# Optimization experiments

Measured on AMD Instinct MI355X. Metric: run time of the kernel, lower is better.

The kernel has to match this reference:

```python
import jax, jax.numpy as jnp
import numpy as np

N = 50000      # nodes
E = 800000     # edges (before self-loops)
IN = 128       # in_channels
HID = 32       # hidden_channels per head
H = 4          # in_head
OUT = 40       # out_channels
OH = 1         # out_head
NEG = 0.2      # GATConv default negative_slope
EPS = 1e-5     # BatchNorm eps
SKIP = 0.5     # skip_coefficient


def setup_inputs() -> dict:
    key = jax.random.key(0)
    ks = jax.random.split(key, 24)
    s = 0.1
    f32 = jnp.float32
    return dict(
        x=jax.random.normal(ks[0], (N, IN), dtype=f32),
        W0=jax.random.normal(ks[1], (H * HID, IN), dtype=f32) * s,
        as0=jax.random.normal(ks[2], (H, HID), dtype=f32) * s,
        ad0=jax.random.normal(ks[3], (H, HID), dtype=f32) * s,
        b0=jnp.zeros((H * HID,), f32),
        g0=jnp.ones((H * HID,), f32),
        be0=jnp.zeros((H * HID,), f32),
        W1=jax.random.normal(ks[4], (H * HID, H * HID), dtype=f32) * s,
        as1=jax.random.normal(ks[5], (H, HID), dtype=f32) * s,
        ad1=jax.random.normal(ks[6], (H, HID), dtype=f32) * s,
        b1=jnp.zeros((H * HID,), f32),
        g1=jnp.ones((H * HID,), f32),
        be1=jnp.zeros((H * HID,), f32),
        W2=jax.random.normal(ks[7], (OH * OUT, H * HID), dtype=f32) * s,
        as2=jax.random.normal(ks[8], (OH, OUT), dtype=f32) * s,
        ad2=jax.random.normal(ks[9], (OH, OUT), dtype=f32) * s,
        b2=jnp.zeros((OH * OUT,), f32),
        edge_index=jax.random.randint(ks[10], (2, E), 0, N, dtype=jnp.int64),
    )


def gat_layer(x, src, dst, W, a_s, a_d, b, heads, ch):
    # PyG GATConv (concat=True): per-head linear, edge LeakyReLU attention,
    # softmax over incoming edges per destination node, scatter-add aggregate.
    n = x.shape[0]
    h = (x @ W.T).reshape(n, heads, ch)            # [N,H,C]
    al_s = jnp.einsum('nhc,hc->nh', h, a_s)        # [N,H]
    al_d = jnp.einsum('nhc,hc->nh', h, a_d)
    e = jax.nn.leaky_relu(al_s[src] + al_d[dst], NEG)   # [Etot,H]
    m = jax.ops.segment_max(e, dst, num_segments=n)     # per-dst max (stable softmax)
    ex = jnp.exp(e - m[dst])
    denom = jax.ops.segment_sum(ex, dst, num_segments=n)
    alpha = ex / denom[dst]                              # [Etot,H]
    out = jax.ops.segment_sum(alpha[:, :, None] * h[src], dst, num_segments=n)
    return out.reshape(n, heads * ch) + b


def batchnorm(x, g, b):
    # BatchNorm1d, batch-statistics form
    mu = x.mean(0)
    var = x.var(0)
    return (x - mu) * jax.lax.rsqrt(var + EPS) * g + b


def reference(x, W0, as0, ad0, b0, g0, be0, W1, as1, ad1, b1, g1, be1,
              W2, as2, ad2, b2, edge_index):
    loops = jnp.arange(N, dtype=edge_index.dtype)   # GATConv add_self_loops=True
    src = jnp.concatenate([edge_index[0], loops])
    dst = jnp.concatenate([edge_index[1], loops])
    h = jax.nn.relu(batchnorm(gat_layer(x, src, dst, W0, as0, ad0, b0, H, HID), g0, be0))
    skip = h
    h = gat_layer(h, src, dst, W1, as1, ad1, b1, H, HID)
    h = jax.nn.relu(batchnorm(h, g1, be1) + SKIP * skip)
    return gat_layer(h, src, dst, W2, as2, ad2, b2, OH, OUT)
```

## Files before the change

### kernel.cpp

```cpp
#include <hip/hip_runtime.h>
#include <hip/hip_bf16.h>
#include <stdint.h>

#define N_NODES 50000
#define N_EDGES 800000
#define TOT_EDGES (N_EDGES + N_NODES)
#define DIM 128
#define NEG 0.2f
#define BN_EPS 1e-5f
#define SKIPC 0.5f
#define NB 196
#define BCAP 6144
#define EPB 2048
#define BINA_BLKS ((N_EDGES + EPB - 1) / EPB)

typedef __attribute__((ext_vector_type(8))) short short8;
typedef __attribute__((ext_vector_type(4))) float f32x4;

__device__ inline float bf2f(__hip_bfloat16 v) { return __bfloat162float(v); }
__device__ inline float u16f(unsigned short u) { return __uint_as_float(((unsigned int)u) << 16); }
__device__ inline unsigned short f2bu(float f) {
    __hip_bfloat16 b = __float2bfloat16(f);
    return *(unsigned short*)&b;
}
__device__ inline void fma8(float* acc, float ex, uint4 u) {
    acc[0] += ex * u16f((unsigned short)(u.x & 0xFFFFu));
    acc[1] += ex * u16f((unsigned short)(u.x >> 16));
    acc[2] += ex * u16f((unsigned short)(u.y & 0xFFFFu));
    acc[3] += ex * u16f((unsigned short)(u.y >> 16));
    acc[4] += ex * u16f((unsigned short)(u.z & 0xFFFFu));
    acc[5] += ex * u16f((unsigned short)(u.z >> 16));
    acc[6] += ex * u16f((unsigned short)(u.w & 0xFFFFu));
    acc[7] += ex * u16f((unsigned short)(u.w >> 16));
}
__device__ inline unsigned int pk2(float a, float b) {
    return (unsigned int)f2bu(a) | ((unsigned int)f2bu(b) << 16);
}

__global__ void zero_out_k(unsigned short* out, int n) {
    int g = blockIdx.x * 256 + threadIdx.x;
    if (g < n) out[g] = 0;
}

__device__ inline void binA_body(int bid, const int* __restrict__ ei,
                                 int* __restrict__ bcnt,
                                 unsigned int* __restrict__ pairs) {
    __shared__ int cnt[NB], base[NB], cur[NB];
    __shared__ int sf;
    int t = threadIdx.x;
    if (t == 0) sf = 0;
    for (int i = t; i < NB; i += 256) cnt[i] = 0;
    __syncthreads();
    if (t < 16 && ei[2 * t + 1] != 0) atomicOr(&sf, 1);
    __syncthreads();
    int f = (sf == 0);
    int b0 = bid * EPB;
    unsigned int pk[8];
    int bk[8];
    #pragma unroll
    for (int j = 0; j < 8; ++j) bk[j] = -1;

    auto handle = [&](int slot, int s, int d) {
        if ((unsigned)d < N_NODES && (unsigned)s < N_NODES) {
            bk[slot] = d >> 8;
            pk[slot] = (unsigned int)s | ((unsigned int)(d & 255) << 16);
            atomicAdd(&cnt[bk[slot]], 1);
        }
    };

    if (f) {
        #pragma unroll
        for (int j = 0; j < 4; ++j) {
            int i0 = b0 + j * 512 + 2 * t;
            if (i0 < N_EDGES) {
                int4 sv = *(const int4*)(ei + 2 * (size_t)i0);
                int4 dv = *(const int4*)(ei + 2 * ((size_t)N_EDGES + i0));
                handle(2 * j, sv.x, dv.x);
                if (i0 + 1 < N_EDGES) handle(2 * j + 1, sv.z, dv.z);
            }
        }
    } else {
        #pragma unroll
        for (int j = 0; j < 8; ++j) {
            int g = b0 + j * 256 + t;
            if (g < N_EDGES) handle(j, ei[g], ei[N_EDGES + g]);
        }
    }
    __syncthreads();
    if (t < NB) {
        int c = cnt[t];
        base[t] = c ? atomicAdd(&bcnt[t], c) : 0;
        cur[t] = 0;
    }
    __syncthreads();
    #pragma unroll
    for (int j = 0; j < 8; ++j) {
        if (bk[j] >= 0) {
            int off = base[bk[j]] + atomicAdd(&cur[bk[j]], 1);
            if (off < BCAP) pairs[(size_t)bk[j] * BCAP + off] = pk[j];
        }
    }
}

struct PrepJobs { const void* src[13]; float* dst[13]; int n[13]; };
__device__ inline void wcvt_body(int bid,
                                 const void* __restrict__ W0,
                                 const void* __restrict__ W1,
                                 const void* __restrict__ W2,
                                 unsigned short* __restrict__ Wb0,
                                 unsigned short* __restrict__ Wb1,
                                 unsigned short* __restrict__ Wb2,
                                 const PrepJobs& jobs,
                                 int* __restrict__ fflag) {
    __shared__ int cs;
    int t = threadIdx.x;
    if (t == 0) cs = 0;
    __syncthreads();
    {
        unsigned int w = ((const unsigned int*)W0)[t];
        float v0 = u16f((unsigned short)(w & 0xFFFFu));
        float a = fabsf(v0);
        int sane = (a < 2.0f && (a > 1e-20f || v0 == 0.0f)) ? 1 : 0;
        atomicAdd(&cs, sane);
    }
    __syncthreads();
    int f = (cs >= 128) ? 1 : 0;
    if (bid == 0 && t == 0) fflag[0] = f;
    if (bid < 148) {
        int g = bid * 256 + t;
        const void* W; unsigned short* Wb; int idx;
        if (g < 16384)        { W = W0; Wb = Wb0; idx = g; }
        else if (g < 32768)   { W = W1; Wb = Wb1; idx = g - 16384; }
        else if (g < 37888)   { W = W2; Wb = Wb2; idx = g - 32768; }
        else return;
        if (f) Wb[idx] = ((const unsigned short*)W)[idx];
        else   Wb[idx] = f2bu(((const float*)W)[idx]);
    } else {
        int j = bid - 148;
        int n = jobs.n[j];
        const void* s = jobs.src[j];
        float* d = jobs.dst[j];
        for (int i = t; i < n; i += 256)
            d[i] = f ? bf2f(((const __hip_bfloat16*)s)[i]) : ((const float*)s)[i];
    }
}

__global__ __launch_bounds__(256) void fat1_k(const int* __restrict__ ei,
                                              int* __restrict__ bcnt,
                                              unsigned int* __restrict__ pairs,
                                              const void* __restrict__ W0,
                                              const void* __restrict__ W1,
                                              const void* __restrict__ W2,
                                              unsigned short* __restrict__ Wb0,
                                              unsigned short* __restrict__ Wb1,
                                              unsigned short* __restrict__ Wb2,
                                              PrepJobs jobs,
                                              int* __restrict__ fflag) {
    if (blockIdx.x < BINA_BLKS) binA_body(blockIdx.x, ei, bcnt, pairs);
    else wcvt_body(blockIdx.x - BINA_BLKS, W0, W1, W2, Wb0, Wb1, Wb2, jobs, fflag);
}

__device__ inline void binB_body(int b, const int* __restrict__ bcnt,
                                 const unsigned int* __restrict__ pairs,
                                 int* __restrict__ row_ptr,
                                 int* __restrict__ ssrc) {
    __shared__ int cntL[256], scanL[256], curL[256];
    __shared__ int sred[256];
    int t = threadIdx.x;
    int n0 = b * 256;
    int nn = min(256, N_NODES - n0);
    int cnt_b = min(bcnt[b], BCAP);
    int contrib = 0;
    if (t < b) contrib = min(bcnt[t], BCAP) + min(256, N_NODES - t * 256);
    sred[t] = contrib;
    __syncthreads();
    #pragma unroll
    for (int off = 128; off > 0; off >>= 1) {
        if (t < off) sred[t] += sred[t + off];
        __syncthreads();
    }
    int gbase = sred[0];
    if (b == NB - 1 && t == 0) row_ptr[N_NODES] = gbase + cnt_b + nn;

    const unsigned int* P = pairs + (size_t)b * BCAP;
    cntL[t] = (t < nn) ? 1 : 0;
    __syncthreads();
    for (int i = t; i < cnt_b; i += 256)
        atomicAdd(&cntL[P[i] >> 16], 1);
    __syncthreads();
    int v = cntL[t];
    scanL[t] = v;
    __syncthreads();
    for (int off = 1; off < 256; off <<= 1) {
        int x = (t >= off) ? scanL[t - off] : 0;
        __syncthreads();
        scanL[t] += x;
        __syncthreads();
    }
    int excl = scanL[t] - v;
    if (t < nn) row_ptr[n0 + t] = gbase + excl;
    curL[t] = excl;
    __syncthreads();
    if (t < nn) {
        int pos = atomicAdd(&curL[t], 1);
        ssrc[gbase + pos] = n0 + t;
    }
    for (int i = t; i < cnt_b; i += 256) {
        unsigned int p = P[i];
        int pos = atomicAdd(&curL[p >> 16], 1);
        ssrc[gbase + pos] = (int)(p & 0xFFFFu);
    }
}

__device__ inline void wext_body(int bid,
                                 unsigned short* __restrict__ Wb0,
                                 unsigned short* __restrict__ Wb1,
                                 unsigned short* __restrict__ Wb2,
                                 const float* __restrict__ pAs0, const float* __restrict__ pAd0,
                                 const float* __restrict__ pAs1, const float* __restrict__ pAd1,
                                 const float* __restrict__ pAs2, const float* __restrict__ pAd2) {
    int g = bid * 256 + threadIdx.x;
    if (g < 2048) {
        int layer = g >> 10;
        int gi = g & 1023;
        int rowq = gi >> 7;
        int k = gi & 127;
        int hh = rowq & 3, dir = rowq >> 2;
        unsigned short* Wb = layer ? Wb1 : Wb0;
        const float* p = layer ? (dir ? pAd1 : pAs1) : (dir ? pAd0 : pAs0);
        float v = 0.f;
        #pragma unroll
        for (int c = 0; c < 32; ++c)
            v += p[hh * 32 + c] * u16f(Wb[(size_t)(hh * 32 + c) * 128 + k]);
        Wb[(size_t)(128 + dir * 4 + hh) * 128 + k] = f2bu(v);
    } else if (g < 2304) {
        int gi = g - 2048;
        int dir = gi >> 7;
        int k = gi & 127;
        const float* p = dir ? pAd2 : pAs2;
        float v = 0.f;
        #pragma unroll
        for (int c = 0; c < 40; ++c)
            v += p[c] * u16f(Wb2[(size_t)c * 128 + k]);
        Wb2[(size_t)(40 + dir) * 128 + k] = f2bu(v);
    }
}

__global__ __launch_bounds__(256) void fat2_k(const int* __restrict__ bcnt,
                                              const unsigned int* __restrict__ pairs,
                                              int* __restrict__ row_ptr,
                                              int* __restrict__ ssrc,
                                              unsigned short* __restrict__ Wb0,
                                              unsigned short* __restrict__ Wb1,
                                              unsigned short* __restrict__ Wb2,
                                              const float* __restrict__ pAs0, const float* __restrict__ pAd0,
                                              const float* __restrict__ pAs1, const float* __restrict__ pAd1,
                                              const float* __restrict__ pAs2, const float* __restrict__ pAd2) {
    if (blockIdx.x < NB) binB_body(blockIdx.x, bcnt, pairs, row_ptr, ssrc);
    else wext_body(blockIdx.x - NB, Wb0, Wb1, Wb2, pAs0, pAd0, pAs1, pAd1, pAs2, pAd2);
}

template<int MT, int MV, int ALBASE, int NH, int AMODE>
__device__ inline void mfma_body(const void* __restrict__ X,
                                 const unsigned short* __restrict__ Xprev,
                                 const unsigned short* __restrict__ Wb,
                                 unsigned short* __restrict__ Y,
                                 float* __restrict__ als, float* __restrict__ ald, int n,
                                 const float* __restrict__ bnA, const float* __restrict__ gA,
                                 const float* __restrict__ beA,
                                 const float* __restrict__ bnB, const float* __restrict__ gB,
                                 const float* __restrict__ beB) {
    const int MROWS = ALBASE + 2 * NH;
    __shared__ float sAsc[128], sAsh[128], sBsc[128], sBsh[128];
    if (AMODE >= 2) {
        int t = threadIdx.x;
        const float invN = 1.f / (float)N_NODES;
        if (t < 128) {
            float mean = bnA[t] * invN;
            float var = fmaxf(bnA[128 + t] * invN - mean * mean, 0.f);
            float s = rsqrtf(var + BN_EPS) * gA[t];
            sAsc[t] = s;
            sAsh[t] = beA[t] - mean * s;
        } else if (AMODE == 3) {
            int c = t - 128;
            float mean = bnB[c] * invN;
            float var = fmaxf(bnB[128 + c] * invN - mean * mean, 0.f);
            float s = rsqrtf(var + BN_EPS) * gB[c];
            sBsc[c] = s;
            sBsh[c] = beB[c] - mean * s;
        }
        __syncthreads();
    }
    int wave = (blockIdx.x * blockDim.x + threadIdx.x) >> 6;
    int r0 = wave * 16;
    if (r0 >= n) return;
    int lane = threadIdx.x & 63;
    int m = lane & 15, quad = lane >> 4;
    f32x4 acc[MT];
    #pragma unroll
    for (int t = 0; t < MT; ++t) acc[t] = (f32x4){0.f, 0.f, 0.f, 0.f};
    int arow = min(r0 + m, n - 1);

    #pragma unroll
    for (int kc = 0; kc < 4; ++kc) {
        int k0 = kc * 32 + quad * 8;
        short8 a;
        if (AMODE == 0) {
            const float* xp = (const float*)X + (size_t)arow * 128 + k0;
            float4 x0 = *(const float4*)xp;
            float4 x1 = *(const float4*)(xp + 4);
            a[0] = (short)f2bu(x0.x); a[1] = (short)f2bu(x0.y);
            a[2] = (short)f2bu(x0.z); a[3] = (short)f2bu(x0.w);
            a[4] = (short)f2bu(x1.x); a[5] = (short)f2bu(x1.y);
            a[6] = (short)f2bu(x1.z); a[7] = (short)f2bu(x1.w);
        } else if (AMODE == 1) {
            a = *(const short8*)((const unsigned short*)X + (size_t)arow * 128 + k0);
        } else if (AMODE == 2) {
            short8 hv = *(const short8*)((const unsigned short*)X + (size_t)arow * 128 + k0);
            #pragma unroll
            for (int j = 0; j < 8; ++j) {
                float v = u16f((unsigned short)hv[j]) * sAsc[k0 + j] + sAsh[k0 + j];
                a[j] = (short)f2bu(fmaxf(v, 0.f));
            }
        } else {
            short8 hv = *(const short8*)((const unsigned short*)X + (size_t)arow * 128 + k0);
            short8 pv = *(const short8*)(Xprev + (size_t)arow * 128 + k0);
            #pragma unroll
            for (int j = 0; j < 8; ++j) {
                float v0 = fmaxf(u16f((unsigned short)pv[j]) * sBsc[k0 + j] + sBsh[k0 + j], 0.f);
                float v = u16f((unsigned short)hv[j]) * sAsc[k0 + j] + sAsh[k0 + j] + SKIPC * v0;
                a[j] = (short)f2bu(fmaxf(v, 0.f));
            }
        }
        #pragma unroll
        for (int t = 0; t < MT; ++t) {
            int col = t * 16 + m;
            short8 b;
            if (col < MROWS) b = *(const short8*)(Wb + (size_t)col * 128 + k0);
            else             b = (short8){0,0,0,0,0,0,0,0};
            acc[t] = __builtin_amdgcn_mfma_f32_16x16x32_bf16(a, b, acc[t], 0, 0, 0);
        }
    }

    #pragma unroll
    for (int t = 0; t < MT; ++t) {
        int col = t * 16 + m;
        #pragma unroll
        for (int r = 0; r < 4; ++r) {
            int row = r0 + quad * 4 + r;
            if (row >= n) continue;
            if (col < MV) {
                Y[(size_t)row * MV + col] = f2bu(acc[t][r]);
            } else if (col < ALBASE + NH) {
                als[row * NH + (col - ALBASE)] = acc[t][r];
            } else if (col < ALBASE + 2 * NH) {
                ald[row * NH + (col - ALBASE - NH)] = acc[t][r];
            }
        }
    }
}

__global__ __launch_bounds__(256) void mfma_x_k(const void* __restrict__ X,
                                                const unsigned short* __restrict__ Wb,
                                                unsigned short* __restrict__ Y,
                                                float* __restrict__ als, float* __restrict__ ald,
                                                int n, const int* __restrict__ fflag) {
    if (fflag[0]) mfma_body<9, 128, 128, 4, 1>(X, nullptr, Wb, Y, als, ald, n,
                                               nullptr, nullptr, nullptr, nullptr, nullptr, nullptr);
    else          mfma_body<9, 128, 128, 4, 0>(X, nullptr, Wb, Y, als, ald, n,
                                               nullptr, nullptr, nullptr, nullptr, nullptr, nullptr);
}

__global__ __launch_bounds__(256) void mfma_aff_k(const unsigned short* __restrict__ X,
                                                  const unsigned short* __restrict__ Wb,
                                                  unsigned short* __restrict__ Y,
                                                  float* __restrict__ als, float* __restrict__ ald,
                                                  int n,
                                                  const float* __restrict__ bn,
                                                  const float* __restrict__ g,
                                                  const float* __restrict__ be) {
    mfma_body<9, 128, 128, 4, 2>(X, nullptr, Wb, Y, als, ald, n,
                                 bn, g, be, nullptr, nullptr, nullptr);
}

__global__ __launch_bounds__(256) void mfma_affskip_k(const unsigned short* __restrict__ X,
                                                      const unsigned short* __restrict__ Xprev,
                                                      const unsigned short* __restrict__ Wb,
                                                      unsigned short* __restrict__ Y,
                                                      float* __restrict__ als, float* __restrict__ ald,
                                                      int n,
                                                      const float* __restrict__ bnA,
                                                      const float* __restrict__ gA,
                                                      const float* __restrict__ beA,
                                                      const float* __restrict__ bnB,
                                                      const float* __restrict__ gB,
                                                      const float* __restrict__ beB) {
    mfma_body<3, 40, 40, 1, 3>(X, Xprev, Wb, Y, als, ald, n,
                               bnA, gA, beA, bnB, gB, beB);
}

template<int H, int C, int LPG, int CPL, bool FINAL>
__global__ __launch_bounds__(256) void agg4_k(const unsigned short* __restrict__ hbuf,
                                              const float* __restrict__ als,
                                              const float* __restrict__ ald,
                                              const float* __restrict__ bias,
                                              const int* __restrict__ row_ptr,
                                              const int* __restrict__ ssrc,
                                              void* __restrict__ out,
                                              const int* __restrict__ fflag, int n) {
    const int HC = H * C;
    const int G = 64 / LPG;
    const int NV = CPL / 8;
    int gw = (blockIdx.x * blockDim.x + threadIdx.x) >> 6;
    if (gw >= n) return;
    int lane = threadIdx.x & 63;
    int grp = lane / LPG;
    int sl  = lane % LPG;
    int c0 = sl * CPL;
    bool act = c0 < HC;
    int hl = act ? (c0 / C) : 0;
    int d = gw;
    int beg = row_ptr[d], end = row_ptr[d + 1];
    float adh = ald[d * H + hl];

    float denom = 0.f;
    float acc[CPL];
    #pragma unroll
    for (int j = 0; j < CPL; ++j) acc[j] = 0.f;

    int i0 = beg + grp;
    bool h0 = i0 < end;
    bool h1 = (i0 + G) < end;
    bool h2 = (i0 + 2 * G) < end;
    float al0 = 0.f, al1 = 0.f, al2 = 0.f;
    uint4 u0[NV], u1[NV], u2[NV];
    if (h0) {
        int s = ssrc[i0];
        al0 = als[s * H + hl];
        if (act) {
            const uint4* hp = (const uint4*)(hbuf + (size_t)s * HC + c0);
            #pragma unroll
            for (int v = 0; v < NV; ++v) u0[v] = hp[v];
        }
    }
    if (h1) {
        int s = ssrc[i0 + G];
        al1 = als[s * H + hl];
        if (act) {
            const uint4* hp = (const uint4*)(hbuf + (size_t)s * HC + c0);
            #pragma unroll
            for (int v = 0; v < NV; ++v) u1[v] = hp[v];
        }
    }
    if (h2) {
        int s = ssrc[i0 + 2 * G];
        al2 = als[s * H + hl];
        if (act) {
            const uint4* hp = (const uint4*)(hbuf + (size_t)s * HC + c0);
            #pragma unroll
            for (int v = 0; v < NV; ++v) u2[v] = hp[v];
        }
    }
    int inext = i0 + 3 * G;

    while (h0) {
        bool h3 = inext < end;
        float al3 = 0.f;
        uint4 u3[NV];
        if (h3) {
            int s = ssrc[inext];
            al3 = als[s * H + hl];
            if (act) {
                const uint4* hp = (const uint4*)(hbuf + (size_t)s * HC + c0);
                #pragma unroll
                for (int v = 0; v < NV; ++v) u3[v] = hp[v];
            }
        }
        float t = al0 + adh;
        t = t > 0.f ? t : NEG * t;
        float ex = __expf(t);
        denom += ex;
        if (act) {
            #pragma unroll
            for (int v = 0; v < NV; ++v) fma8(acc + v * 8, ex, u0[v]);
        }
        h0 = h1; al0 = al1;
        #pragma unroll
        for (int v = 0; v < NV; ++v) u0[v] = u1[v];
        h1 = h2; al1 = al2;
        #pragma unroll
        for (int v = 0; v < NV; ++v) u1[v] = u2[v];
        h2 = h3; al2 = al3;
        #pragma unroll
        for (int v = 0; v < NV; ++v) u2[v] = u3[v];
        inext += G;
    }

    #pragma unroll
    for (int off = LPG; off < 64; off <<= 1) {
        denom += __shfl_xor(denom, off, 64);
        #pragma unroll
        for (int j = 0; j < CPL; ++j) acc[j] += __shfl_xor(acc[j], off, 64);
    }

    if (grp == 0 && act) {
        float inv = 1.f / denom;
        float vals[CPL];
        #pragma unroll
        for (int j = 0; j < CPL; ++j) vals[j] = acc[j] * inv + bias[c0 + j];
        if (FINAL && !fflag[0]) {
            float* of = (float*)out + (size_t)d * HC + c0;
            #pragma unroll
            for (int j = 0; j < CPL; ++j) of[j] = vals[j];
        } else {
            unsigned short* ob = (unsigned short*)out + (size_t)d * HC + c0;
            #pragma unroll
            for (int v = 0; v < NV; ++v) {
                uint4 pk;
                pk.x = pk2(vals[v * 8 + 0], vals[v * 8 + 1]);
                pk.y = pk2(vals[v * 8 + 2], vals[v * 8 + 3]);
                pk.z = pk2(vals[v * 8 + 4], vals[v * 8 + 5]);
                pk.w = pk2(vals[v * 8 + 6], vals[v * 8 + 7]);
                *(uint4*)(ob + v * 8) = pk;
            }
        }
    }
}

__global__ __launch_bounds__(256) void bn_stats_k(const unsigned short* __restrict__ x,
                                                  float* __restrict__ sum,
                                                  float* __restrict__ sumsq, int n) {
    __shared__ float ss[128], sq[128];
    int t = threadIdx.x;
    int rt = t >> 4;
    int c8 = (t & 15) * 8;
    float s[8], q[8];
    #pragma unroll
    for (int j = 0; j < 8; ++j) { s[j] = 0.f; q[j] = 0.f; }
    for (int r = blockIdx.x * 16 + rt; r < n; r += gridDim.x * 16) {
        short8 v = *(const short8*)(x + (size_t)r * 128 + c8);
        #pragma unroll
        for (int j = 0; j < 8; ++j) {
            float f = u16f((unsigned short)v[j]);
            s[j] += f; q[j] += f * f;
        }
    }
    if (t < 128) { ss[t] = 0.f; sq[t] = 0.f; }
    __syncthreads();
    #pragma unroll
    for (int j = 0; j < 8; ++j) {
        atomicAdd(&ss[c8 + j], s[j]);
        atomicAdd(&sq[c8 + j], q[j]);
    }
    __syncthreads();
    if (t < 128) {
        atomicAdd(&sum[t], ss[t]);
        atomicAdd(&sumsq[t], sq[t]);
    }
}

extern "C" void kernel_launch(void* const* d_in, const int* in_sizes, int n_in,
                              void* d_out, int out_size, void* d_ws, size_t ws_size,
                              hipStream_t stream) {
    const void* x   = d_in[0];
    const void* W0  = d_in[1];
    const void* as0 = d_in[2];
    const void* ad0 = d_in[3];
    const void* b0  = d_in[4];
    const void* g0  = d_in[5];
    const void* be0 = d_in[6];
    const void* W1  = d_in[7];
    const void* as1 = d_in[8];
    const void* ad1 = d_in[9];
    const void* b1  = d_in[10];
    const void* g1  = d_in[11];
    const void* be1 = d_in[12];
    const void* W2  = d_in[13];
    const void* as2 = d_in[14];
    const void* ad2 = d_in[15];
    const void* b2  = d_in[16];
    const int* ei = (const int*)d_in[17];

    char* w = (char*)d_ws;
    size_t off = 0;
    auto alloc = [&](size_t bytes) -> void* {
        void* p = w + off;
        off = (off + bytes + 255) & ~(size_t)255;
        return p;
    };
    unsigned short* hbf = (unsigned short*)alloc((size_t)N_NODES * 128 * 2);
    unsigned short* hA0 = (unsigned short*)alloc((size_t)N_NODES * 128 * 2);
    unsigned short* hA1 = (unsigned short*)alloc((size_t)N_NODES * 128 * 2);
    float* als = (float*)alloc((size_t)N_NODES * 4 * 4);
    float* ald = (float*)alloc((size_t)N_NODES * 4 * 4);
    unsigned short* Wb0 = (unsigned short*)alloc((size_t)136 * 128 * 2);
    unsigned short* Wb1 = (unsigned short*)alloc((size_t)136 * 128 * 2);
    unsigned short* Wb2 = (unsigned short*)alloc((size_t)42 * 128 * 2);
    float* prm = (float*)alloc(2048 * 4);
    int* zreg = (int*)alloc((size_t)(NB + 512) * 4);
    int* bcnt = zreg;
    float* bn0 = (float*)(zreg + NB);
    float* bn1 = bn0 + 256;
    int* row_ptr = (int*)alloc((size_t)(N_NODES + 1) * 4);
    int* ssrc    = (int*)alloc((size_t)TOT_EDGES * 4);
    unsigned int* pairs = (unsigned int*)alloc((size_t)NB * BCAP * 4);
    int* fflag   = (int*)alloc(256);

    float* pAs0 = prm + 0,   * pAd0 = prm + 128,  * pB0 = prm + 256;
    float* pG0  = prm + 384, * pBe0 = prm + 512;
    float* pAs1 = prm + 640, * pAd1 = prm + 768,  * pB1 = prm + 896;
    float* pG1  = prm + 1024,* pBe1 = prm + 1152;
    float* pAs2 = prm + 1280,* pAd2 = prm + 1320, * pB2 = prm + 1360;

    if (off > ws_size) {
        zero_out_k<<<(out_size + 255) / 256, 256, 0, stream>>>((unsigned short*)d_out, out_size);
        return;
    }

    const int MB = (((N_NODES + 15) / 16) + 3) / 4;
    const int AB = (N_NODES * 64 + 255) / 256;

    PrepJobs jobs;
    const void* srcs[13] = { as0, ad0, b0, g0, be0, as1, ad1, b1, g1, be1, as2, ad2, b2 };
    float* dsts[13] = { pAs0, pAd0, pB0, pG0, pBe0, pAs1, pAd1, pB1, pG1, pBe1, pAs2, pAd2, pB2 };
    int ns[13] = { 128,128,128,128,128, 128,128,128,128,128, 40,40,40 };
    for (int i = 0; i < 13; ++i) { jobs.src[i] = srcs[i]; jobs.dst[i] = dsts[i]; jobs.n[i] = ns[i]; }

    hipMemsetAsync(zreg, 0, (size_t)(NB + 512) * 4, stream);
    fat1_k<<<BINA_BLKS + 161, 256, 0, stream>>>(ei, bcnt, pairs, W0, W1, W2, Wb0, Wb1, Wb2, jobs, fflag);
    fat2_k<<<NB + 9, 256, 0, stream>>>(bcnt, pairs, row_ptr, ssrc, Wb0, Wb1, Wb2,
                                       pAs0, pAd0, pAs1, pAd1, pAs2, pAd2);
    mfma_x_k<<<MB, 256, 0, stream>>>(x, Wb0, hbf, als, ald, N_NODES, fflag);
    agg4_k<4, 32, 8, 16, false><<<AB, 256, 0, stream>>>(hbf, als, ald, pB0, row_ptr, ssrc, hA0, fflag, N_NODES);
    bn_stats_k<<<256, 256, 0, stream>>>(hA0, bn0, bn0 + 128, N_NODES);
    mfma_aff_k<<<MB, 256, 0, stream>>>(hA0, Wb1, hbf, als, ald, N_NODES, bn0, pG0, pBe0);
    agg4_k<4, 32, 8, 16, false><<<AB, 256, 0, stream>>>(hbf, als, ald, pB1, row_ptr, ssrc, hA1, fflag, N_NODES);
    bn_stats_k<<<256, 256, 0, stream>>>(hA1, bn1, bn1 + 128, N_NODES);
    mfma_affskip_k<<<MB, 256, 0, stream>>>(hA1, hA0, Wb2, hbf, als, ald, N_NODES,
                                           bn1, pG1, pBe1, bn0, pG0, pBe0);
    agg4_k<1, 40, 8, 8, true><<<AB, 256, 0, stream>>>(hbf, als, ald, pB2, row_ptr, ssrc, d_out, fflag, N_NODES);
}
```

Measured before the change: 323.7 us.

## Fuse prep, bn-stats and GEMM stages into cooperative kernels with grid sync

Replaces the memset, the two prep kernels and the first GEMM with one cooperative kernel that uses grid.sync between phases. It also fuses each bn_stats launch with the following GEMM through a grid barrier. GEMM work becomes a grid-stride job loop so a persistent grid sized to occupancy can cover every row. The aim is to cut kernel launch and inter-kernel drain overhead, at the cost of grid barriers, reduced parallelism in the single-block prep phases, and a fallback path for when cooperative launch fails.

```diff
diff --git a/kernel.cpp b/kernel.cpp
--- a/kernel.cpp
+++ b/kernel.cpp
@@ -1,6 +1,9 @@
 #include <hip/hip_runtime.h>
 #include <hip/hip_bf16.h>
+#include <hip/hip_cooperative_groups.h>
 #include <stdint.h>
+
+namespace cg = cooperative_groups;
 
 #define N_NODES 50000
 #define N_EDGES 800000
@@ -13,6 +16,8 @@
 #define BCAP 6144
 #define EPB 2048
 #define BINA_BLKS ((N_EDGES + EPB - 1) / EPB)
+#define GEMM_JOBS ((N_NODES + 63) >> 6)
+#define ZN (NB + 512)
 
 typedef __attribute__((ext_vector_type(8))) short short8;
 typedef __attribute__((ext_vector_type(4))) float f32x4;
@@ -145,21 +150,6 @@
     }
 }
 
-__global__ __launch_bounds__(256) void fat1_k(const int* __restrict__ ei,
-                                              int* __restrict__ bcnt,
-                                              unsigned int* __restrict__ pairs,
-                                              const void* __restrict__ W0,
-                                              const void* __restrict__ W1,
-                                              const void* __restrict__ W2,
-                                              unsigned short* __restrict__ Wb0,
-                                              unsigned short* __restrict__ Wb1,
-                                              unsigned short* __restrict__ Wb2,
-                                              PrepJobs jobs,
-                                              int* __restrict__ fflag) {
-    if (blockIdx.x < BINA_BLKS) binA_body(blockIdx.x, ei, bcnt, pairs);
-    else wcvt_body(blockIdx.x - BINA_BLKS, W0, W1, W2, Wb0, Wb1, Wb2, jobs, fflag);
-}
-
 __device__ inline void binB_body(int b, const int* __restrict__ bcnt,
                                  const unsigned int* __restrict__ pairs,
                                  int* __restrict__ row_ptr,
@@ -246,30 +236,17 @@
     }
 }
 
-__global__ __launch_bounds__(256) void fat2_k(const int* __restrict__ bcnt,
-                                              const unsigned int* __restrict__ pairs,
-                                              int* __restrict__ row_ptr,
-                                              int* __restrict__ ssrc,
-                                              unsigned short* __restrict__ Wb0,
-                                              unsigned short* __restrict__ Wb1,
-                                              unsigned short* __restrict__ Wb2,
-                                              const float* __restrict__ pAs0, const float* __restrict__ pAd0,
-                                              const float* __restrict__ pAs1, const float* __restrict__ pAd1,
-                                              const float* __restrict__ pAs2, const float* __restrict__ pAd2) {
-    if (blockIdx.x < NB) binB_body(blockIdx.x, bcnt, pairs, row_ptr, ssrc);
-    else wext_body(blockIdx.x - NB, Wb0, Wb1, Wb2, pAs0, pAd0, pAs1, pAd1, pAs2, pAd2);
-}
-
 template<int MT, int MV, int ALBASE, int NH, int AMODE>
-__device__ inline void mfma_body(const void* __restrict__ X,
-                                 const unsigned short* __restrict__ Xprev,
-                                 const unsigned short* __restrict__ Wb,
-                                 unsigned short* __restrict__ Y,
-                                 float* __restrict__ als, float* __restrict__ ald, int n,
-                                 const float* __restrict__ bnA, const float* __restrict__ gA,
-                                 const float* __restrict__ beA,
-                                 const float* __restrict__ bnB, const float* __restrict__ gB,
-                                 const float* __restrict__ beB) {
+__device__ inline void gemm_phase(int bid, int nblk,
+                                  const void* __restrict__ X,
+                                  const unsigned short* __restrict__ Xprev,
+                                  const unsigned short* __restrict__ Wb,
+                                  unsigned short* __restrict__ Y,
+                                  float* __restrict__ als, float* __restrict__ ald, int n,
+                                  const float* __restrict__ bnA, const float* __restrict__ gA,
+                                  const float* __restrict__ beA,
+                                  const float* __restrict__ bnB, const float* __restrict__ gB,
+                                  const float* __restrict__ beB) {
     const int MROWS = ALBASE + 2 * NH;
     __shared__ float sAsc[128], sAsh[128], sBsc[128], sBsh[128];
     if (AMODE >= 2) {
@@ -291,73 +268,203 @@
         }
         __syncthreads();
     }
-    int wave = (blockIdx.x * blockDim.x + threadIdx.x) >> 6;
-    int r0 = wave * 16;
-    if (r0 >= n) return;
     int lane = threadIdx.x & 63;
     int m = lane & 15, quad = lane >> 4;
-    f32x4 acc[MT];
-    #pragma unroll
-    for (int t = 0; t < MT; ++t) acc[t] = (f32x4){0.f, 0.f, 0.f, 0.f};
-    int arow = min(r0 + m, n - 1);
-
-    #pragma unroll
-    for (int kc = 0; kc < 4; ++kc) {
-        int k0 = kc * 32 + quad * 8;
-        short8 a;
-        if (AMODE == 0) {
-            const float* xp = (const float*)X + (size_t)arow * 128 + k0;
-            float4 x0 = *(const float4*)xp;
-            float4 x1 = *(const float4*)(xp + 4);
-            a[0] = (short)f2bu(x0.x); a[1] = (short)f2bu(x0.y);
-            a[2] = (short)f2bu(x0.z); a[3] = (short)f2bu(x0.w);
-            a[4] = (short)f2bu(x1.x); a[5] = (short)f2bu(x1.y);
-            a[6] = (short)f2bu(x1.z); a[7] = (short)f2bu(x1.w);
-        } else if (AMODE == 1) {
-            a = *(const short8*)((const unsigned short*)X + (size_t)arow * 128 + k0);
-        } else if (AMODE == 2) {
-            short8 hv = *(const short8*)((const unsigned short*)X + (size_t)arow * 128 + k0);
+    int wl = threadIdx.x >> 6;
+    const int JOBS = (n + 63) >> 6;
+    for (int job = bid; job < JOBS; job += nblk) {
+        int r0 = (job << 6) + (wl << 4);
+        if (r0 >= n) continue;
+        f32x4 acc[MT];
+        #pragma unroll
+        for (int t = 0; t < MT; ++t) acc[t] = (f32x4){0.f, 0.f, 0.f, 0.f};
+        int arow = min(r0 + m, n - 1);
+
+        #pragma unroll
+        for (int kc = 0; kc < 4; ++kc) {
+            int k0 = kc * 32 + quad * 8;
+            short8 a;
+            if (AMODE == 0) {
+                const float* xp = (const float*)X + (size_t)arow * 128 + k0;
+                float4 x0 = *(const float4*)xp;
+                float4 x1 = *(const float4*)(xp + 4);
+                a[0] = (short)f2bu(x0.x); a[1] = (short)f2bu(x0.y);
+                a[2] = (short)f2bu(x0.z); a[3] = (short)f2bu(x0.w);
+                a[4] = (short)f2bu(x1.x); a[5] = (short)f2bu(x1.y);
+                a[6] = (short)f2bu(x1.z); a[7] = (short)f2bu(x1.w);
+            } else if (AMODE == 1) {
+                a = *(const short8*)((const unsigned short*)X + (size_t)arow * 128 + k0);
+            } else if (AMODE == 2) {
+                short8 hv = *(const short8*)((const unsigned short*)X + (size_t)arow * 128 + k0);
+                #pragma unroll
+                for (int j = 0; j < 8; ++j) {
+                    float v = u16f((unsigned short)hv[j]) * sAsc[k0 + j] + sAsh[k0 + j];
+                    a[j] = (short)f2bu(fmaxf(v, 0.f));
+                }
+            } else {
+                short8 hv = *(const short8*)((const unsigned short*)X + (size_t)arow * 128 + k0);
+                short8 pv = *(const short8*)(Xprev + (size_t)arow * 128 + k0);
+                #pragma unroll
+                for (int j = 0; j < 8; ++j) {
+                    float v0 = fmaxf(u16f((unsigned short)pv[j]) * sBsc[k0 + j] + sBsh[k0 + j], 0.f);
+                    float v = u16f((unsigned short)hv[j]) * sAsc[k0 + j] + sAsh[k0 + j] + SKIPC * v0;
+                    a[j] = (short)f2bu(fmaxf(v, 0.f));
+                }
+            }
             #pragma unroll
-            for (int j = 0; j < 8; ++j) {
-                float v = u16f((unsigned short)hv[j]) * sAsc[k0 + j] + sAsh[k0 + j];
-                a[j] = (short)f2bu(fmaxf(v, 0.f));
+            for (int t = 0; t < MT; ++t) {
+                int col = t * 16 + m;
+                short8 b;
+                if (col < MROWS) b = *(const short8*)(Wb + (size_t)col * 128 + k0);
+                else             b = (short8){0,0,0,0,0,0,0,0};
+                acc[t] = __builtin_amdgcn_mfma_f32_16x16x32_bf16(a, b, acc[t], 0, 0, 0);
             }
-        } else {
-            short8 hv = *(const short8*)((const unsigned short*)X + (size_t)arow * 128 + k0);
-            short8 pv = *(const short8*)(Xprev + (size_t)arow * 128 + k0);
-            #pragma unroll
-            for (int j = 0; j < 8; ++j) {
-                float v0 = fmaxf(u16f((unsigned short)pv[j]) * sBsc[k0 + j] + sBsh[k0 + j], 0.f);
-                float v = u16f((unsigned short)hv[j]) * sAsc[k0 + j] + sAsh[k0 + j] + SKIPC * v0;
-                a[j] = (short)f2bu(fmaxf(v, 0.f));
-            }
-        }
+        }
+
         #pragma unroll
         for (int t = 0; t < MT; ++t) {
             int col = t * 16 + m;
-            short8 b;
-            if (col < MROWS) b = *(const short8*)(Wb + (size_t)col * 128 + k0);
-            else             b = (short8){0,0,0,0,0,0,0,0};
-            acc[t] = __builtin_amdgcn_mfma_f32_16x16x32_bf16(a, b, acc[t], 0, 0, 0);
-        }
-    }
-
+            #pragma unroll
+            for (int r = 0; r < 4; ++r) {
+                int row = r0 + quad * 4 + r;
+                if (row >= n) continue;
+                if (col < MV) {
+                    Y[(size_t)row * MV + col] = f2bu(acc[t][r]);
+                } else if (col < ALBASE + NH) {
+                    als[row * NH + (col - ALBASE)] = acc[t][r];
+                } else if (col < ALBASE + 2 * NH) {
+                    ald[row * NH + (col - ALBASE - NH)] = acc[t][r];
+                }
+            }
+        }
+    }
+}
+
+__device__ inline void bn_stats_body(int vbid, int vgrid,
+                                     const unsigned short* __restrict__ x,
+                                     float* __restrict__ sum,
+                                     float* __restrict__ sumsq, int n) {
+    __shared__ float ss[128], sq[128];
+    int t = threadIdx.x;
+    int rt = t >> 4;
+    int c8 = (t & 15) * 8;
+    float s[8], q[8];
     #pragma unroll
-    for (int t = 0; t < MT; ++t) {
-        int col = t * 16 + m;
-        #pragma unroll
-        for (int r = 0; r < 4; ++r) {
-            int row = r0 + quad * 4 + r;
-            if (row >= n) continue;
-            if (col < MV) {
-                Y[(size_t)row * MV + col] = f2bu(acc[t][r]);
-            } else if (col < ALBASE + NH) {
-                als[row * NH + (col - ALBASE)] = acc[t][r];
-            } else if (col < ALBASE + 2 * NH) {
-                ald[row * NH + (col - ALBASE - NH)] = acc[t][r];
-            }
-        }
-    }
+    for (int j = 0; j < 8; ++j) { s[j] = 0.f; q[j] = 0.f; }
+    for (int r = vbid * 16 + rt; r < n; r += vgrid * 16) {
+        short8 v = *(const short8*)(x + (size_t)r * 128 + c8);
+        #pragma unroll
+        for (int j = 0; j < 8; ++j) {
+            float f = u16f((unsigned short)v[j]);
+            s[j] += f; q[j] += f * f;
+        }
+    }
+    if (t < 128) { ss[t] = 0.f; sq[t] = 0.f; }
+    __syncthreads();
+    #pragma unroll
+    for (int j = 0; j < 8; ++j) {
+        atomicAdd(&ss[c8 + j], s[j]);
+        atomicAdd(&sq[c8 + j], q[j]);
+    }
+    __syncthreads();
+    if (t < 128) {
+        atomicAdd(&sum[t], ss[t]);
+        atomicAdd(&sumsq[t], sq[t]);
+    }
+}
+
+struct M1Args {
+    const int* ei; int* bcnt; unsigned int* pairs;
+    const void* W0; const void* W1; const void* W2;
+    unsigned short* Wb0; unsigned short* Wb1; unsigned short* Wb2;
+    PrepJobs jobs; int* fflag;
+    int* zreg;
+    int* row_ptr; int* ssrc;
+    const float* pAs0; const float* pAd0; const float* pAs1; const float* pAd1;
+    const float* pAs2; const float* pAd2;
+    const void* X; unsigned short* Y; float* als; float* ald; int n;
+};
+
+__global__ __launch_bounds__(256) void mega1_k(M1Args a) {
+    cg::grid_group grid = cg::this_grid();
+    int bid = blockIdx.x, nblk = gridDim.x;
+    for (int i = bid * 256 + threadIdx.x; i < ZN; i += nblk * 256) a.zreg[i] = 0;
+    grid.sync();
+    for (int job = bid; job < BINA_BLKS + 161; job += nblk) {
+        if (job < BINA_BLKS) binA_body(job, a.ei, a.bcnt, a.pairs);
+        else wcvt_body(job - BINA_BLKS, a.W0, a.W1, a.W2, a.Wb0, a.Wb1, a.Wb2, a.jobs, a.fflag);
+    }
+    grid.sync();
+    for (int job = bid; job < NB + 9; job += nblk) {
+        if (job < NB) binB_body(job, a.bcnt, a.pairs, a.row_ptr, a.ssrc);
+        else wext_body(job - NB, a.Wb0, a.Wb1, a.Wb2, a.pAs0, a.pAd0, a.pAs1, a.pAd1, a.pAs2, a.pAd2);
+    }
+    grid.sync();
+    int f = a.fflag[0];
+    if (f) gemm_phase<9, 128, 128, 4, 1>(bid, nblk, a.X, nullptr, a.Wb0, a.Y, a.als, a.ald, a.n,
+                                         nullptr, nullptr, nullptr, nullptr, nullptr, nullptr);
+    else   gemm_phase<9, 128, 128, 4, 0>(bid, nblk, a.X, nullptr, a.Wb0, a.Y, a.als, a.ald, a.n,
+                                         nullptr, nullptr, nullptr, nullptr, nullptr, nullptr);
+}
+
+struct M2Args {
+    const unsigned short* Xs; float* sum; float* sumsq;
+    const unsigned short* X; const unsigned short* Wb; unsigned short* Y;
+    float* als; float* ald; int n;
+    const float* bn; const float* g; const float* be;
+};
+
+__global__ __launch_bounds__(256) void mega2_k(M2Args a) {
+    cg::grid_group grid = cg::this_grid();
+    if (blockIdx.x < 256) bn_stats_body(blockIdx.x, 256, a.Xs, a.sum, a.sumsq, a.n);
+    grid.sync();
+    gemm_phase<9, 128, 128, 4, 2>(blockIdx.x, gridDim.x, a.X, nullptr, a.Wb, a.Y, a.als, a.ald, a.n,
+                                  a.bn, a.g, a.be, nullptr, nullptr, nullptr);
+}
+
+struct M3Args {
+    const unsigned short* Xs; float* sum; float* sumsq;
+    const unsigned short* X; const unsigned short* Xprev; const unsigned short* Wb;
+    unsigned short* Y; float* als; float* ald; int n;
+    const float* bnA; const float* gA; const float* beA;
+    const float* bnB; const float* gB; const float* beB;
+};
+
+__global__ __launch_bounds__(256) void mega3_k(M3Args a) {
+    cg::grid_group grid = cg::this_grid();
+    if (blockIdx.x < 256) bn_stats_body(blockIdx.x, 256, a.Xs, a.sum, a.sumsq, a.n);
+    grid.sync();
+    gemm_phase<3, 40, 40, 1, 3>(blockIdx.x, gridDim.x, a.X, a.Xprev, a.Wb, a.Y, a.als, a.ald, a.n,
+                                a.bnA, a.gA, a.beA, a.bnB, a.gB, a.beB);
+}
+
+__global__ __launch_bounds__(256) void fat1_k(const int* __restrict__ ei,
+                                              int* __restrict__ bcnt,
+                                              unsigned int* __restrict__ pairs,
+                                              const void* __restrict__ W0,
+                                              const void* __restrict__ W1,
+                                              const void* __restrict__ W2,
+                                              unsigned short* __restrict__ Wb0,
+                                              unsigned short* __restrict__ Wb1,
+                                              unsigned short* __restrict__ Wb2,
+                                              PrepJobs jobs,
+                                              int* __restrict__ fflag) {
+    if (blockIdx.x < BINA_BLKS) binA_body(blockIdx.x, ei, bcnt, pairs);
+    else wcvt_body(blockIdx.x - BINA_BLKS, W0, W1, W2, Wb0, Wb1, Wb2, jobs, fflag);
+}
+
+__global__ __launch_bounds__(256) void fat2_k(const int* __restrict__ bcnt,
+                                              const unsigned int* __restrict__ pairs,
+                                              int* __restrict__ row_ptr,
+                                              int* __restrict__ ssrc,
+                                              unsigned short* __restrict__ Wb0,
+                                              unsigned short* __restrict__ Wb1,
+                                              unsigned short* __restrict__ Wb2,
+                                              const float* __restrict__ pAs0, const float* __restrict__ pAd0,
+                                              const float* __restrict__ pAs1, const float* __restrict__ pAd1,
+                                              const float* __restrict__ pAs2, const float* __restrict__ pAd2) {
+    if (blockIdx.x < NB) binB_body(blockIdx.x, bcnt, pairs, row_ptr, ssrc);
+    else wext_body(blockIdx.x - NB, Wb0, Wb1, Wb2, pAs0, pAd0, pAs1, pAd1, pAs2, pAd2);
 }
 
 __global__ __launch_bounds__(256) void mfma_x_k(const void* __restrict__ X,
@@ -365,10 +472,10 @@
                                                 unsigned short* __restrict__ Y,
                                                 float* __restrict__ als, float* __restrict__ ald,
                                                 int n, const int* __restrict__ fflag) {
-    if (fflag[0]) mfma_body<9, 128, 128, 4, 1>(X, nullptr, Wb, Y, als, ald, n,
-                                               nullptr, nullptr, nullptr, nullptr, nullptr, nullptr);
-    else          mfma_body<9, 128, 128, 4, 0>(X, nullptr, Wb, Y, als, ald, n,
-                                               nullptr, nullptr, nullptr, nullptr, nullptr, nullptr);
+    if (fflag[0]) gemm_phase<9, 128, 128, 4, 1>(blockIdx.x, gridDim.x, X, nullptr, Wb, Y, als, ald, n,
+                                                nullptr, nullptr, nullptr, nullptr, nullptr, nullptr);
+    else          gemm_phase<9, 128, 128, 4, 0>(blockIdx.x, gridDim.x, X, nullptr, Wb, Y, als, ald, n,
+                                                nullptr, nullptr, nullptr, nullptr, nullptr, nullptr);
 }
 
 __global__ __launch_bounds__(256) void mfma_aff_k(const unsigned short* __restrict__ X,
@@ -379,8 +486,8 @@
                                                   const float* __restrict__ bn,
                                                   const float* __restrict__ g,
                                                   const float* __restrict__ be) {
-    mfma_body<9, 128, 128, 4, 2>(X, nullptr, Wb, Y, als, ald, n,
-                                 bn, g, be, nullptr, nullptr, nullptr);
+    gemm_phase<9, 128, 128, 4, 2>(blockIdx.x, gridDim.x, X, nullptr, Wb, Y, als, ald, n,
+                                  bn, g, be, nullptr, nullptr, nullptr);
 }
 
 __global__ __launch_bounds__(256) void mfma_affskip_k(const unsigned short* __restrict__ X,
@@ -395,8 +502,14 @@
                                                       const float* __restrict__ bnB,
                                                       const float* __restrict__ gB,
                                                       const float* __restrict__ beB) {
-    mfma_body<3, 40, 40, 1, 3>(X, Xprev, Wb, Y, als, ald, n,
-                               bnA, gA, beA, bnB, gB, beB);
+    gemm_phase<3, 40, 40, 1, 3>(blockIdx.x, gridDim.x, X, Xprev, Wb, Y, als, ald, n,
+                                bnA, gA, beA, bnB, gB, beB);
+}
+
+__global__ __launch_bounds__(256) void bn_stats_k(const unsigned short* __restrict__ x,
+                                                  float* __restrict__ sum,
+                                                  float* __restrict__ sumsq, int n) {
+    bn_stats_body(blockIdx.x, gridDim.x, x, sum, sumsq, n);
 }
 
 template<int H, int C, int LPG, int CPL, bool FINAL>
@@ -527,38 +640,6 @@
     }
 }
 
-__global__ __launch_bounds__(256) void bn_stats_k(const unsigned short* __restrict__ x,
-                                                  float* __restrict__ sum,
-                                                  float* __restrict__ sumsq, int n) {
-    __shared__ float ss[128], sq[128];
-    int t = threadIdx.x;
-    int rt = t >> 4;
-    int c8 = (t & 15) * 8;
-    float s[8], q[8];
-    #pragma unroll
-    for (int j = 0; j < 8; ++j) { s[j] = 0.f; q[j] = 0.f; }
-    for (int r = blockIdx.x * 16 + rt; r < n; r += gridDim.x * 16) {
-        short8 v = *(const short8*)(x + (size_t)r * 128 + c8);
-        #pragma unroll
-        for (int j = 0; j < 8; ++j) {
-            float f = u16f((unsigned short)v[j]);
-            s[j] += f; q[j] += f * f;
-        }
-    }
-    if (t < 128) { ss[t] = 0.f; sq[t] = 0.f; }
-    __syncthreads();
-    #pragma unroll
-    for (int j = 0; j < 8; ++j) {
-        atomicAdd(&ss[c8 + j], s[j]);
-        atomicAdd(&sq[c8 + j], q[j]);
-    }
-    __syncthreads();
-    if (t < 128) {
-        atomicAdd(&sum[t], ss[t]);
-        atomicAdd(&sumsq[t], sq[t]);
-    }
-}
-
 extern "C" void kernel_launch(void* const* d_in, const int* in_sizes, int n_in,
                               void* d_out, int out_size, void* d_ws, size_t ws_size,
                               hipStream_t stream) {
@@ -597,7 +678,7 @@
     unsigned short* Wb1 = (unsigned short*)alloc((size_t)136 * 128 * 2);
     unsigned short* Wb2 = (unsigned short*)alloc((size_t)42 * 128 * 2);
     float* prm = (float*)alloc(2048 * 4);
-    int* zreg = (int*)alloc((size_t)(NB + 512) * 4);
+    int* zreg = (int*)alloc((size_t)ZN * 4);
     int* bcnt = zreg;
     float* bn0 = (float*)(zreg + NB);
     float* bn1 = bn0 + 256;
@@ -617,7 +698,7 @@
         return;
     }
 
-    const int MB = (((N_NODES + 15) / 16) + 3) / 4;
+    const int MB = GEMM_JOBS;
     const int AB = (N_NODES * 64 + 255) / 256;
 
     PrepJobs jobs;
@@ -626,17 +707,86 @@
     int ns[13] = { 128,128,128,128,128, 128,128,128,128,128, 40,40,40 };
     for (int i = 0; i < 13; ++i) { jobs.src[i] = srcs[i]; jobs.dst[i] = dsts[i]; jobs.n[i] = ns[i]; }
 
-    hipMemsetAsync(zreg, 0, (size_t)(NB + 512) * 4, stream);
-    fat1_k<<<BINA_BLKS + 161, 256, 0, stream>>>(ei, bcnt, pairs, W0, W1, W2, Wb0, Wb1, Wb2, jobs, fflag);
-    fat2_k<<<NB + 9, 256, 0, stream>>>(bcnt, pairs, row_ptr, ssrc, Wb0, Wb1, Wb2,
-                                       pAs0, pAd0, pAs1, pAd1, pAs2, pAd2);
-    mfma_x_k<<<MB, 256, 0, stream>>>(x, Wb0, hbf, als, ald, N_NODES, fflag);
+    static int s_init = 0, s_cu = 0, s_o1 = 0, s_o2 = 0, s_o3 = 0;
+    static int s_coop = -1;
+    if (!s_init) {
+        hipDeviceProp_t prop;
+        if (hipGetDeviceProperties(&prop, 0) == hipSuccess) s_cu = prop.multiProcessorCount;
+        (void)hipOccupancyMaxActiveBlocksPerMultiprocessor(&s_o1, mega1_k, 256, 0);
+        (void)hipOccupancyMaxActiveBlocksPerMultiprocessor(&s_o2, mega2_k, 256, 0);
+        (void)hipOccupancyMaxActiveBlocksPerMultiprocessor(&s_o3, mega3_k, 256, 0);
+        s_init = 1;
+    }
+    bool tryCoop = (s_coop != 0) && s_cu > 0 && s_o1 > 0 && s_o2 > 0 && s_o3 > 0;
+
+    bool done = false;
+    if (tryCoop) {
+        M1Args a1;
+        a1.ei = ei; a1.bcnt = bcnt; a1.pairs = pairs;
+        a1.W0 = W0; a1.W1 = W1; a1.W2 = W2;
+        a1.Wb0 = Wb0; a1.Wb1 = Wb1; a1.Wb2 = Wb2;
+        a1.jobs = jobs; a1.fflag = fflag;
+        a1.zreg = zreg;
+        a1.row_ptr = row_ptr; a1.ssrc = ssrc;
+        a1.pAs0 = pAs0; a1.pAd0 = pAd0; a1.pAs1 = pAs1; a1.pAd1 = pAd1;
+        a1.pAs2 = pAs2; a1.pAd2 = pAd2;
+        a1.X = x; a1.Y = hbf; a1.als = als; a1.ald = ald; a1.n = N_NODES;
+        void* p1[] = { (void*)&a1 };
+        int g1 = s_cu * s_o1; if (g1 > GEMM_JOBS) g1 = GEMM_JOBS;
+        if (hipLaunchCooperativeKernel((const void*)mega1_k, dim3(g1), dim3(256), p1, 0, stream) == hipSuccess)
+            done = true;
+        else { (void)hipGetLastError(); s_coop = 0; tryCoop = false; }
+    }
+    if (!done) {
+        hipMemsetAsync(zreg, 0, (size_t)ZN * 4, stream);
+        fat1_k<<<BINA_BLKS + 161, 256, 0, stream>>>(ei, bcnt, pairs, W0, W1, W2, Wb0, Wb1, Wb2, jobs, fflag);
+        fat2_k<<<NB + 9, 256, 0, stream>>>(bcnt, pairs, row_ptr, ssrc, Wb0, Wb1, Wb2,
+                                           pAs0, pAd0, pAs1, pAd1, pAs2, pAd2);
+        mfma_x_k<<<MB, 256, 0, stream>>>(x, Wb0, hbf, als, ald, N_NODES, fflag);
+    }
+
     agg4_k<4, 32, 8, 16, false><<<AB, 256, 0, stream>>>(hbf, als, ald, pB0, row_ptr, ssrc, hA0, fflag, N_NODES);
-    bn_stats_k<<<256, 256, 0, stream>>>(hA0, bn0, bn0 + 128, N_NODES);
-    mfma_aff_k<<<MB, 256, 0, stream>>>(hA0, Wb1, hbf, als, ald, N_NODES, bn0, pG0, pBe0);
+
+    done = false;
+    if (tryCoop) {
+        M2Args a2;
+        a2.Xs = hA0; a2.sum = bn0; a2.sumsq = bn0 + 128;
+        a2.X = hA0; a2.Wb = Wb1; a2.Y = hbf;
+        a2.als = als; a2.ald = ald; a2.n = N_NODES;
+        a2.bn = bn0; a2.g = pG0; a2.be = pBe0;
+        void* p2[] = { (void*)&a2 };
+        int g2 = s_cu * s_o2; if (g2 > GEMM_JOBS) g2 = GEMM_JOBS;
+        if (hipLaunchCooperativeKernel((const void*)mega2_k, dim3(g2), dim3(256), p2, 0, stream) == hipSuccess)
+            done = true;
+        else { (void)hipGetLastError(); s_coop = 0; tryCoop = false; }
+    }
+    if (!done) {
+        bn_stats_k<<<256, 256, 0, stream>>>(hA0, bn0, bn0 + 128, N_NODES);
+        mfma_aff_k<<<MB, 256, 0, stream>>>(hA0, Wb1, hbf, als, ald, N_NODES, bn0, pG0, pBe0);
+    }
+
     agg4_k<4, 32, 8, 16, false><<<AB, 256, 0, stream>>>(hbf, als, ald, pB1, row_ptr, ssrc, hA1, fflag, N_NODES);
-    bn_stats_k<<<256, 256, 0, stream>>>(hA1, bn1, bn1 + 128, N_NODES);
-    mfma_affskip_k<<<MB, 256, 0, stream>>>(hA1, hA0, Wb2, hbf, als, ald, N_NODES,
-                                           bn1, pG1, pBe1, bn0, pG0, pBe0);
+
+    done = false;
+    if (tryCoop) {
+        M3Args a3;
+        a3.Xs = hA1; a3.sum = bn1; a3.sumsq = bn1 + 128;
+        a3.X = hA1; a3.Xprev = hA0; a3.Wb = Wb2; a3.Y = hbf;
+        a3.als = als; a3.ald = ald; a3.n = N_NODES;
+        a3.bnA = bn1; a3.gA = pG1; a3.beA = pBe1;
+        a3.bnB = bn0; a3.gB = pG0; a3.beB = pBe0;
+        void* p3[] = { (void*)&a3 };
+        int g3 = s_cu * s_o3; if (g3 > GEMM_JOBS) g3 = GEMM_JOBS;
+        if (hipLaunchCooperativeKernel((const void*)mega3_k, dim3(g3), dim3(256), p3, 0, stream) == hipSuccess)
+            done = true;
+        else { (void)hipGetLastError(); s_coop = 0; }
+    }
+    if (!done) {
+        bn_stats_k<<<256, 256, 0, stream>>>(hA1, bn1, bn1 + 128, N_NODES);
+        mfma_affskip_k<<<MB, 256, 0, stream>>>(hA1, hA0, Wb2, hbf, als, ald, N_NODES,
+                                               bn1, pG1, pBe1, bn0, pG0, pBe0);
+    }
+    if (s_coop == -1 && tryCoop) s_coop = 1;
+
     agg4_k<1, 40, 8, 8, true><<<AB, 256, 0, stream>>>(hbf, als, ald, pB2, row_ptr, ssrc, d_out, fflag, N_NODES);
 }
```

After: 517.6 us. +59.9%, slower.
